# Performance work log

Measured on AMD Instinct MI355X. Metric: run time of the kernel, lower is better.

The kernel has to match this reference:

```python
import jax, jax.numpy as jnp
import numpy as np

B, H, W, D, K = 64, 32, 32, 64, 512


def setup_inputs() -> dict:
    key = jax.random.key(0)
    k1, k2 = jax.random.split(key)
    x = jax.random.normal(k1, (B, H, W, D), dtype=jnp.float32)
    # tf.random_uniform_initializer default: U(-0.05, 0.05)
    embeddings = jax.random.uniform(k2, (D, K), dtype=jnp.float32,
                                    minval=-0.05, maxval=0.05)
    return {"x": x, "embeddings": embeddings}


def reference(x, embeddings):
    # embeddings: [D, K] (columns are codebook vectors)
    d = embeddings.shape[0]
    flat = x.reshape(-1, d)  # [N, D]
    # squared L2 distance to each code: ||z||^2 + ||e||^2 - 2 z.e
    distances = (jnp.sum(flat * flat, axis=1, keepdims=True)
                 + jnp.sum(embeddings * embeddings, axis=0)
                 - 2.0 * flat @ embeddings)  # [N, K]
    encoding_indices = jnp.argmin(distances, axis=1)  # [N]
    # one-hot @ embeddings^T  ==  gather of codebook rows
    quantized = jnp.take(embeddings.T, encoding_indices, axis=0).reshape(x.shape)
    sg = jax.lax.stop_gradient
    commitment_loss = jnp.mean((sg(quantized) - x) ** 2)  # commitment_cost = 1
    codebook_loss = jnp.mean((quantized - sg(x)) ** 2)
    loss = commitment_loss + codebook_loss
    out = x + sg(quantized - x)  # straight-through estimator
    return out, loss
```

## Files before the change

### kernel.cpp

```cpp
#include <hip/hip_runtime.h>

#define NVEC 65536
#define DIM 64
#define KCODES 512
#define VPB 128
#define NBLK 512
#define ELS 2048.0f
#define INV_ELS (1.0f / 2048.0f)
#define GAP_THR 2e-4f

typedef _Float16 f16x8 __attribute__((ext_vector_type(8)));
typedef float    f32x4 __attribute__((ext_vector_type(4)));

#define WS_EN   4
#define WS_EH   1024
#define WS_EL   (1024 + 16384)
#define WS_PART 33792
#define WS_EMBT 34816

__global__ __launch_bounds__(512, 1) void prep_kernel(const float* __restrict__ emb,
                                                      float* __restrict__ ws) {
    const int tid = threadIdx.x;
    const int b   = blockIdx.x;
    if (b == 0) {
        float s = 0.f;
#pragma unroll
        for (int d = 0; d < DIM; ++d) { float v = emb[d * KCODES + tid]; s = fmaf(v, v, s); }
        ws[WS_EN + tid] = s;
    } else if (b <= 8) {
        const int fl = (b - 1) * 512 + tid;
        const int ct = fl >> 7, s5 = (fl >> 6) & 1, l = fl & 63;
        const int k  = ct * 16 + (l & 15);
        const int d0 = s5 * 32 + (l >> 4) * 8;
        f16x8 eh, el;
#pragma unroll
        for (int e = 0; e < 8; ++e) {
            float v = emb[(d0 + e) * KCODES + k];
            _Float16 h = (_Float16)v;
            _Float16 l16 = (_Float16)((v - (float)h) * ELS);
            eh[e] = -(h + h);
            el[e] = -(l16 + l16);
        }
        ((f16x8*)(ws + WS_EH))[fl] = eh;
        ((f16x8*)(ws + WS_EL))[fl] = el;
    } else {
        __shared__ float tl[64][65];
        const int kt = b - 9;
        const int r  = tid >> 3;
        const int g  = tid & 7;
#pragma unroll
        for (int i = 0; i < 8; ++i)
            tl[r][g * 8 + i] = emb[r * KCODES + kt * 64 + g * 8 + i];
        __syncthreads();
#pragma unroll
        for (int i = 0; i < 8; ++i)
            ws[WS_EMBT + (kt * 64 + r) * 64 + g * 8 + i] = tl[g * 8 + i][r];
    }
}

__global__ __launch_bounds__(512, 2) void vq_kernel(const float* __restrict__ x,
                                                    const float* __restrict__ ws_ro,
                                                    float* __restrict__ out,
                                                    float* __restrict__ part) {
    __shared__ f16x8 zhS[VPB][8];
    __shared__ f16x8 zlS[VPB][8];
    __shared__ float enS[KCODES];
    __shared__ int   cand[VPB][2];
    __shared__ float sdfm[VPB][2];
    __shared__ float exd[VPB][2];
    __shared__ int   bksel[VPB];
    __shared__ float swl[8];

    const int tid  = threadIdx.x;
    const int wid  = tid >> 6;
    const int lane = tid & 63;
    const size_t xbase = (size_t)blockIdx.x * VPB * DIM;

    enS[tid] = ws_ro[WS_EN + tid];

    {
        const int v  = tid >> 2;
        const int d0 = (tid & 3) * 16;
        const float* xp = x + xbase + v * DIM + d0;
        float4 a = *(const float4*)(xp);
        float4 b = *(const float4*)(xp + 4);
        float4 c = *(const float4*)(xp + 8);
        float4 e = *(const float4*)(xp + 12);
        float t0[8] = {a.x, a.y, a.z, a.w, b.x, b.y, b.z, b.w};
        float t1[8] = {c.x, c.y, c.z, c.w, e.x, e.y, e.z, e.w};
        f16x8 h0, l0, h1, l1;
#pragma unroll
        for (int i = 0; i < 8; ++i) {
            _Float16 h = (_Float16)t0[i]; h0[i] = h; l0[i] = (_Float16)((t0[i] - (float)h) * ELS);
            _Float16 g = (_Float16)t1[i]; h1[i] = g; l1[i] = (_Float16)((t1[i] - (float)g) * ELS);
        }
        const int u0 = ((d0 >> 3))     ^ (v & 7);
        const int u1 = ((d0 >> 3) + 1) ^ (v & 7);
        zhS[v][u0] = h0; zhS[v][u1] = h1;
        zlS[v][u0] = l0; zlS[v][u1] = l1;
    }
    __syncthreads();

    const int vb = wid * 16;
    const int r  = lane & 15;
    const int g4 = lane >> 4;
    const int vA = vb + r;
    const int sw = vA & 7;
    f16x8 ah0 = zhS[vA][(g4)     ^ sw];
    f16x8 ah1 = zhS[vA][(4 + g4) ^ sw];
    f16x8 al0 = zlS[vA][(g4)     ^ sw];
    f16x8 al1 = zlS[vA][(4 + g4) ^ sw];

    const f16x8* ehp = (const f16x8*)(ws_ro + WS_EH);
    const f16x8* elp = (const f16x8*)(ws_ro + WS_EL);

    float best[4]  = {3.4e38f, 3.4e38f, 3.4e38f, 3.4e38f};
    float best2[4] = {3.4e38f, 3.4e38f, 3.4e38f, 3.4e38f};
    int   bk1[4]   = {0, 0, 0, 0};
    int   bk2[4]   = {0, 0, 0, 0};

    f16x8 Ah0 = ehp[lane],        Ah1 = ehp[64 + lane];
    f16x8 Al0 = elp[lane],        Al1 = elp[64 + lane];
    f16x8 Bh0 = ehp[128 + lane],  Bh1 = ehp[192 + lane];
    f16x8 Bl0 = elp[128 + lane],  Bl1 = elp[192 + lane];

#define COMPUTE(T, H0, H1, L0, L1) { \
        const float enk = enS[(T) * 16 + r]; \
        f32x4 acch = {enk, enk, enk, enk}; \
        f32x4 accm = {0.f, 0.f, 0.f, 0.f}; \
        acch = __builtin_amdgcn_mfma_f32_16x16x32_f16(ah0, H0, acch, 0, 0, 0); \
        acch = __builtin_amdgcn_mfma_f32_16x16x32_f16(ah1, H1, acch, 0, 0, 0); \
        accm = __builtin_amdgcn_mfma_f32_16x16x32_f16(al0, H0, accm, 0, 0, 0); \
        accm = __builtin_amdgcn_mfma_f32_16x16x32_f16(al1, H1, accm, 0, 0, 0); \
        accm = __builtin_amdgcn_mfma_f32_16x16x32_f16(ah0, L0, accm, 0, 0, 0); \
        accm = __builtin_amdgcn_mfma_f32_16x16x32_f16(ah1, L1, accm, 0, 0, 0); \
        const int kk = (T) * 16 + r; \
        _Pragma("unroll") \
        for (int j = 0; j < 4; ++j) { \
            float sc = fmaf(accm[j], INV_ELS, acch[j]); \
            bool c1 = sc < best[j]; \
            bool c2 = sc < best2[j]; \
            bk2[j]   = c1 ? bk1[j] : (c2 ? kk : bk2[j]); \
            bk1[j]   = c1 ? kk : bk1[j]; \
            best2[j] = __builtin_amdgcn_fmed3f(sc, best[j], best2[j]); \
            best[j]  = fminf(sc, best[j]); \
        } }

#pragma unroll 1
    for (int ct = 0; ct < 32; ct += 2) {
        f16x8 nAh0, nAh1, nAl0, nAl1, nBh0, nBh1, nBl0, nBl1;
        if (ct < 30) {
            const int o = (ct + 2) * 128 + lane;
            nAh0 = ehp[o]; nAh1 = ehp[o + 64];
            nAl0 = elp[o]; nAl1 = elp[o + 64];
        }
        COMPUTE(ct, Ah0, Ah1, Al0, Al1)
        if (ct < 30) {
            const int o = (ct + 3) * 128 + lane;
            nBh0 = ehp[o]; nBh1 = ehp[o + 64];
            nBl0 = elp[o]; nBl1 = elp[o + 64];
        }
        COMPUTE(ct + 1, Bh0, Bh1, Bl0, Bl1)
        if (ct < 30) {
            Ah0 = nAh0; Ah1 = nAh1; Al0 = nAl0; Al1 = nAl1;
            Bh0 = nBh0; Bh1 = nBh1; Bl0 = nBl0; Bl1 = nBl1;
        }
    }
#undef COMPUTE

#pragma unroll
    for (int m = 1; m <= 8; m <<= 1) {
#pragma unroll
        for (int j = 0; j < 4; ++j) {
            float qb  = __shfl_xor(best[j],  m);
            int   qk  = __shfl_xor(bk1[j],   m);
            float q2  = __shfl_xor(best2[j], m);
            int   qk2 = __shfl_xor(bk2[j],   m);
            bool  t1  = (qb < best[j]) || (qb == best[j] && qk < bk1[j]);
            float lb  = t1 ? best[j] : qb;
            int   lk  = t1 ? bk1[j]  : qk;
            float nb  = t1 ? qb : best[j];
            int   nk  = t1 ? qk : bk1[j];
            bool  ta  = (best2[j] < q2) || (best2[j] == q2 && bk2[j] < qk2);
            float sb  = ta ? best2[j] : q2;
            int   sk  = ta ? bk2[j]   : qk2;
            bool  tb  = (lb < sb) || (lb == sb && lk < sk);
            best2[j]  = tb ? lb : sb;
            bk2[j]    = tb ? lk : sk;
            best[j]   = nb;
            bk1[j]    = nk;
        }
    }
    {
        const int j = lane & 15;
        if (j < 4) {
            const int v = vb + g4 * 4 + j;
            sdfm[v][0] = j == 0 ? best[0]  : j == 1 ? best[1]  : j == 2 ? best[2]  : best[3];
            sdfm[v][1] = j == 0 ? best2[0] : j == 1 ? best2[1] : j == 2 ? best2[2] : best2[3];
            cand[v][0] = j == 0 ? bk1[0]   : j == 1 ? bk1[1]   : j == 2 ? bk1[2]   : bk1[3];
            cand[v][1] = j == 0 ? bk2[0]   : j == 1 ? bk2[1]   : j == 2 ? bk2[2]   : bk2[3];
        }
    }
    __syncthreads();

    if (tid < 2 * VPB) {
        const int v = tid >> 1, cc = tid & 1;
        float res = sdfm[v][cc];
        if (sdfm[v][1] - sdfm[v][0] <= GAP_THR) {
            const int k = cand[v][cc];
            const float* xr = x + xbase + v * DIM;
            const float* er = ws_ro + WS_EMBT + k * 64;
            float zn = 0.f, dot = 0.f;
#pragma unroll
            for (int d = 0; d < DIM; ++d) {
                float xv = xr[d];
                zn  = fmaf(xv, xv, zn);
                dot = fmaf(xv, er[d], dot);
            }
            res = fmaf(-2.0f, dot, zn + enS[k]);
        }
        exd[v][cc] = res;
    }
    __syncthreads();
    if (tid < VPB) {
        const int k0 = cand[tid][0], k1 = cand[tid][1];
        const float d0 = exd[tid][0], d1 = exd[tid][1];
        const bool take2 = (d1 < d0) || (d1 == d0 && k1 < k0);
        bksel[tid] = take2 ? k1 : k0;
    }
    __syncthreads();

    const int v16 = tid >> 2;
    const int j16 = (tid & 3) * 16;
    const int bk  = bksel[v16];
    const int gvec = blockIdx.x * VPB + v16;
    const float*  xg  = x + (size_t)gvec * DIM + j16;
    float*        og  = out + (size_t)gvec * DIM + j16;
    const float4* et4 = (const float4*)(ws_ro + WS_EMBT + bk * 64);

    float lossLocal = 0.f;
#pragma unroll
    for (int c = 0; c < 4; ++c) {
        float4 q  = et4[(tid & 3) * 4 + c];
        *(float4*)(og + c * 4) = q;
        float4 xa = *(const float4*)(xg + c * 4);
        float a;
        a = q.x - xa.x; lossLocal = fmaf(a, a, lossLocal);
        a = q.y - xa.y; lossLocal = fmaf(a, a, lossLocal);
        a = q.z - xa.z; lossLocal = fmaf(a, a, lossLocal);
        a = q.w - xa.w; lossLocal = fmaf(a, a, lossLocal);
    }

#pragma unroll
    for (int off = 32; off; off >>= 1) lossLocal += __shfl_down(lossLocal, off, 64);
    if (lane == 0) swl[wid] = lossLocal;
    __syncthreads();
    if (tid == 0) {
        float s = 0.f;
#pragma unroll
        for (int i = 0; i < 8; ++i) s += swl[i];
        part[WS_PART + blockIdx.x] = s;
    }
}

__global__ __launch_bounds__(256, 1) void finish_kernel(const float* __restrict__ part,
                                                        float* __restrict__ out) {
    __shared__ float sw[4];
    const int tid = threadIdx.x, lane = tid & 63, wid = tid >> 6;
    float s = part[WS_PART + tid] + part[WS_PART + tid + 256];
#pragma unroll
    for (int off = 32; off; off >>= 1) s += __shfl_down(s, off, 64);
    if (lane == 0) sw[wid] = s;
    __syncthreads();
    if (tid == 0) {
        float total = sw[0] + sw[1] + sw[2] + sw[3];
        out[(size_t)NVEC * DIM] = 2.0f * total / (float)((size_t)NVEC * DIM);
    }
}

extern "C" void kernel_launch(void* const* d_in, const int* in_sizes, int n_in,
                              void* d_out, int out_size, void* d_ws, size_t ws_size,
                              hipStream_t stream) {
    const float* x   = (const float*)d_in[0];
    const float* emb = (const float*)d_in[1];
    float* out = (float*)d_out;
    float* ws  = (float*)d_ws;

    prep_kernel<<<dim3(17), dim3(512), 0, stream>>>(emb, ws);
    vq_kernel<<<dim3(NBLK), dim3(512), 0, stream>>>(x, ws, out, ws);
    finish_kernel<<<dim3(1), dim3(256), 0, stream>>>(ws, out);
}
```

Measured before the change: 45.44 us.

## Pack score and tile index into biased uint keys for min-tracking

Adds a positive bias to code norms so scores stay positive, then packs the float bits with the tile index in the low 5 mantissa bits. This replaces the float/index select chains of the top-2 update with unsigned min/max. The cross-lane reduction now shuffles packed 64-bit keys, and the low-mantissa accumulation is split across two independent MFMA chains. The next-tile prefetch is simplified and now reads past the last tile on the final iteration. Truncating the mantissa coarsens the scores, which the slightly wider exact-recheck gap threshold is meant to cover.

Result: faster. 39.11 us (-13.9%).

```diff
diff --git a/kernel.cpp b/kernel.cpp
--- a/kernel.cpp
+++ b/kernel.cpp
@@ -7,10 +7,12 @@
 #define NBLK 512
 #define ELS 2048.0f
 #define INV_ELS (1.0f / 2048.0f)
-#define GAP_THR 2e-4f
+#define BIAS 8.0f
+#define GAP_THR 2.5e-4f
 
 typedef _Float16 f16x8 __attribute__((ext_vector_type(8)));
 typedef float    f32x4 __attribute__((ext_vector_type(4)));
+typedef unsigned long long u64;
 
 #define WS_EN   4
 #define WS_EH   1024
@@ -64,7 +66,7 @@
                                                     float* __restrict__ part) {
     __shared__ f16x8 zhS[VPB][8];
     __shared__ f16x8 zlS[VPB][8];
-    __shared__ float enS[KCODES];
+    __shared__ float enS8[KCODES];
     __shared__ int   cand[VPB][2];
     __shared__ float sdfm[VPB][2];
     __shared__ float exd[VPB][2];
@@ -76,7 +78,7 @@
     const int lane = tid & 63;
     const size_t xbase = (size_t)blockIdx.x * VPB * DIM;
 
-    enS[tid] = ws_ro[WS_EN + tid];
+    enS8[tid] = ws_ro[WS_EN + tid] + BIAS;
 
     {
         const int v  = tid >> 2;
@@ -101,11 +103,11 @@
     }
     __syncthreads();
 
-    const int vb = wid * 16;
-    const int r  = lane & 15;
-    const int g4 = lane >> 4;
-    const int vA = vb + r;
-    const int sw = vA & 7;
+    const int vb  = wid * 16;
+    const int col = lane & 15;
+    const int g4  = lane >> 4;
+    const int vA  = vb + col;
+    const int sw  = vA & 7;
     f16x8 ah0 = zhS[vA][(g4)     ^ sw];
     f16x8 ah1 = zhS[vA][(4 + g4) ^ sw];
     f16x8 al0 = zlS[vA][(g4)     ^ sw];
@@ -114,91 +116,75 @@
     const f16x8* ehp = (const f16x8*)(ws_ro + WS_EH);
     const f16x8* elp = (const f16x8*)(ws_ro + WS_EL);
 
-    float best[4]  = {3.4e38f, 3.4e38f, 3.4e38f, 3.4e38f};
-    float best2[4] = {3.4e38f, 3.4e38f, 3.4e38f, 3.4e38f};
-    int   bk1[4]   = {0, 0, 0, 0};
-    int   bk2[4]   = {0, 0, 0, 0};
+    unsigned b1[4] = {~0u, ~0u, ~0u, ~0u};
+    unsigned b2[4] = {~0u, ~0u, ~0u, ~0u};
 
     f16x8 Ah0 = ehp[lane],        Ah1 = ehp[64 + lane];
     f16x8 Al0 = elp[lane],        Al1 = elp[64 + lane];
     f16x8 Bh0 = ehp[128 + lane],  Bh1 = ehp[192 + lane];
     f16x8 Bl0 = elp[128 + lane],  Bl1 = elp[192 + lane];
+    int onx = 256 + lane;
 
 #define COMPUTE(T, H0, H1, L0, L1) { \
-        const float enk = enS[(T) * 16 + r]; \
-        f32x4 acch = {enk, enk, enk, enk}; \
-        f32x4 accm = {0.f, 0.f, 0.f, 0.f}; \
-        acch = __builtin_amdgcn_mfma_f32_16x16x32_f16(ah0, H0, acch, 0, 0, 0); \
-        acch = __builtin_amdgcn_mfma_f32_16x16x32_f16(ah1, H1, acch, 0, 0, 0); \
-        accm = __builtin_amdgcn_mfma_f32_16x16x32_f16(al0, H0, accm, 0, 0, 0); \
-        accm = __builtin_amdgcn_mfma_f32_16x16x32_f16(al1, H1, accm, 0, 0, 0); \
-        accm = __builtin_amdgcn_mfma_f32_16x16x32_f16(ah0, L0, accm, 0, 0, 0); \
-        accm = __builtin_amdgcn_mfma_f32_16x16x32_f16(ah1, L1, accm, 0, 0, 0); \
-        const int kk = (T) * 16 + r; \
+        const float enk8 = enS8[(T) * 16 + col]; \
+        f32x4 acch  = {enk8, enk8, enk8, enk8}; \
+        f32x4 accm1 = {0.f, 0.f, 0.f, 0.f}; \
+        f32x4 accm2 = {0.f, 0.f, 0.f, 0.f}; \
+        acch  = __builtin_amdgcn_mfma_f32_16x16x32_f16(ah0, H0, acch,  0, 0, 0); \
+        acch  = __builtin_amdgcn_mfma_f32_16x16x32_f16(ah1, H1, acch,  0, 0, 0); \
+        accm1 = __builtin_amdgcn_mfma_f32_16x16x32_f16(al0, H0, accm1, 0, 0, 0); \
+        accm1 = __builtin_amdgcn_mfma_f32_16x16x32_f16(ah0, L0, accm1, 0, 0, 0); \
+        accm2 = __builtin_amdgcn_mfma_f32_16x16x32_f16(al1, H1, accm2, 0, 0, 0); \
+        accm2 = __builtin_amdgcn_mfma_f32_16x16x32_f16(ah1, L1, accm2, 0, 0, 0); \
         _Pragma("unroll") \
         for (int j = 0; j < 4; ++j) { \
-            float sc = fmaf(accm[j], INV_ELS, acch[j]); \
-            bool c1 = sc < best[j]; \
-            bool c2 = sc < best2[j]; \
-            bk2[j]   = c1 ? bk1[j] : (c2 ? kk : bk2[j]); \
-            bk1[j]   = c1 ? kk : bk1[j]; \
-            best2[j] = __builtin_amdgcn_fmed3f(sc, best[j], best2[j]); \
-            best[j]  = fminf(sc, best[j]); \
+            float scb = fmaf(accm1[j] + accm2[j], INV_ELS, acch[j]); \
+            unsigned u = (__float_as_uint(scb) & 0xFFFFFFE0u) | (unsigned)(T); \
+            b2[j] = min(b2[j], max(u, b1[j])); \
+            b1[j] = min(b1[j], u); \
         } }
 
 #pragma unroll 1
     for (int ct = 0; ct < 32; ct += 2) {
-        f16x8 nAh0, nAh1, nAl0, nAl1, nBh0, nBh1, nBl0, nBl1;
-        if (ct < 30) {
-            const int o = (ct + 2) * 128 + lane;
-            nAh0 = ehp[o]; nAh1 = ehp[o + 64];
-            nAl0 = elp[o]; nAl1 = elp[o + 64];
-        }
         COMPUTE(ct, Ah0, Ah1, Al0, Al1)
-        if (ct < 30) {
-            const int o = (ct + 3) * 128 + lane;
-            nBh0 = ehp[o]; nBh1 = ehp[o + 64];
-            nBl0 = elp[o]; nBl1 = elp[o + 64];
-        }
+        Ah0 = ehp[onx]; Ah1 = ehp[onx + 64];
+        Al0 = elp[onx]; Al1 = elp[onx + 64];
         COMPUTE(ct + 1, Bh0, Bh1, Bl0, Bl1)
-        if (ct < 30) {
-            Ah0 = nAh0; Ah1 = nAh1; Al0 = nAl0; Al1 = nAl1;
-            Bh0 = nBh0; Bh1 = nBh1; Bl0 = nBl0; Bl1 = nBl1;
-        }
+        Bh0 = ehp[onx + 128]; Bh1 = ehp[onx + 192];
+        Bl0 = elp[onx + 128]; Bl1 = elp[onx + 192];
+        onx += 256;
     }
 #undef COMPUTE
 
+    u64 q1[4], q2[4];
+#pragma unroll
+    for (int j = 0; j < 4; ++j) {
+        q1[j] = ((u64)(b1[j] & 0xFFFFFFE0u) << 32) | (unsigned)((b1[j] & 31u) * 16 + col);
+        q2[j] = ((u64)(b2[j] & 0xFFFFFFE0u) << 32) | (unsigned)((b2[j] & 31u) * 16 + col);
+    }
 #pragma unroll
     for (int m = 1; m <= 8; m <<= 1) {
 #pragma unroll
         for (int j = 0; j < 4; ++j) {
-            float qb  = __shfl_xor(best[j],  m);
-            int   qk  = __shfl_xor(bk1[j],   m);
-            float q2  = __shfl_xor(best2[j], m);
-            int   qk2 = __shfl_xor(bk2[j],   m);
-            bool  t1  = (qb < best[j]) || (qb == best[j] && qk < bk1[j]);
-            float lb  = t1 ? best[j] : qb;
-            int   lk  = t1 ? bk1[j]  : qk;
-            float nb  = t1 ? qb : best[j];
-            int   nk  = t1 ? qk : bk1[j];
-            bool  ta  = (best2[j] < q2) || (best2[j] == q2 && bk2[j] < qk2);
-            float sb  = ta ? best2[j] : q2;
-            int   sk  = ta ? bk2[j]   : qk2;
-            bool  tb  = (lb < sb) || (lb == sb && lk < sk);
-            best2[j]  = tb ? lb : sb;
-            bk2[j]    = tb ? lk : sk;
-            best[j]   = nb;
-            bk1[j]    = nk;
+            u64 qa = __shfl_xor(q1[j], m);
+            u64 qb = __shfl_xor(q2[j], m);
+            u64 lo = q1[j] < qa ? q1[j] : qa;
+            u64 hi = q1[j] < qa ? qa : q1[j];
+            u64 s2 = q2[j] < qb ? q2[j] : qb;
+            q1[j] = lo;
+            q2[j] = hi < s2 ? hi : s2;
         }
     }
     {
         const int j = lane & 15;
         if (j < 4) {
             const int v = vb + g4 * 4 + j;
-            sdfm[v][0] = j == 0 ? best[0]  : j == 1 ? best[1]  : j == 2 ? best[2]  : best[3];
-            sdfm[v][1] = j == 0 ? best2[0] : j == 1 ? best2[1] : j == 2 ? best2[2] : best2[3];
-            cand[v][0] = j == 0 ? bk1[0]   : j == 1 ? bk1[1]   : j == 2 ? bk1[2]   : bk1[3];
-            cand[v][1] = j == 0 ? bk2[0]   : j == 1 ? bk2[1]   : j == 2 ? bk2[2]   : bk2[3];
+            u64 s1 = j == 0 ? q1[0] : j == 1 ? q1[1] : j == 2 ? q1[2] : q1[3];
+            u64 s2 = j == 0 ? q2[0] : j == 1 ? q2[1] : j == 2 ? q2[2] : q2[3];
+            sdfm[v][0] = __uint_as_float((unsigned)(s1 >> 32));
+            sdfm[v][1] = __uint_as_float((unsigned)(s2 >> 32));
+            cand[v][0] = (int)(s1 & 0x1FFu);
+            cand[v][1] = (int)(s2 & 0x1FFu);
         }
     }
     __syncthreads();
@@ -217,7 +203,7 @@
                 zn  = fmaf(xv, xv, zn);
                 dot = fmaf(xv, er[d], dot);
             }
-            res = fmaf(-2.0f, dot, zn + enS[k]);
+            res = fmaf(-2.0f, dot, zn + ws_ro[WS_EN + k]);
         }
         exd[v][cc] = res;
     }
```
